# Kernel optimization log

Hardware: AMD Instinct MI355X
Metric: run time of the kernel (lower is better)

The kernel has to match this reference:

```python
import jax, jax.numpy as jnp
import numpy as np

N_NODES = 100000
F_DIM = 128      # graph.num_node_features
TE_DIM = 32      # te_emb_dim
D = F_DIM + TE_DIM  # attention embed_dim = 160
B = 4096         # number of target nodes (batched python loop)
K = 64           # candidates per target
TAU = 1.0
THRESHOLD = 0.2
EPS = 1e-10


def setup_inputs() -> dict:
    key = jax.random.key(0)
    ks = jax.random.split(key, 16)
    inp = {
        "x": jax.random.normal(ks[0], (N_NODES, F_DIM), dtype=jnp.float32),
        "target_node_ids": jax.random.randint(ks[1], (B,), 0, N_NODES),
        "target_node_times": jax.random.randint(ks[2], (B,), 1, 10000),
        "neighbor_ids": jax.random.randint(ks[3], (B, K), 0, N_NODES),
        "edge_time": jax.random.randint(ks[4], (B, K), 0, 10000),
        "edge_weight": jax.random.uniform(ks[5], (B, K), dtype=jnp.float32),
        "gumbel_u": jax.random.uniform(ks[6], (B, K), dtype=jnp.float32),
        # TemporalEncoding params: te(t) = cos(t * w + b)
        "te_w": jax.random.normal(ks[7], (TE_DIM,), dtype=jnp.float32),
        "te_b": jax.random.normal(ks[8], (TE_DIM,), dtype=jnp.float32),
        # MultiheadAttention params (packed qkv like torch)
        "in_proj_w": jax.random.normal(ks[9], (3 * D, D), dtype=jnp.float32) / np.sqrt(D),
        "in_proj_b": jnp.zeros((3 * D,), dtype=jnp.float32),
        "out_w": jax.random.normal(ks[10], (D, D), dtype=jnp.float32) / np.sqrt(D),
        "out_b": jnp.zeros((D,), dtype=jnp.float32),
        # MLP: Linear(D+1 -> 1) + LeakyReLU
        "mlp_w": jax.random.normal(ks[11], (D + 1,), dtype=jnp.float32) / np.sqrt(D + 1),
        "mlp_b": jnp.zeros((1,), dtype=jnp.float32),
    }
    return inp


def reference(x, target_node_ids, target_node_times, neighbor_ids, edge_time,
              edge_weight, gumbel_u, te_w, te_b, in_proj_w, in_proj_b,
              out_w, out_b, mlp_w, mlp_b):
    # --- build target embedding: [B, D]
    t_x = x[target_node_ids]                                          # [B, F]
    t_te = jnp.cos(target_node_times[:, None].astype(jnp.float32) * te_w + te_b)  # [B, TE]
    q_in = jnp.concatenate([t_x, t_te], axis=-1)                      # [B, D]

    # --- candidate embeddings: [B, K, D]
    c_x = x[neighbor_ids]                                             # [B, K, F]
    c_te = jnp.cos(edge_time[..., None].astype(jnp.float32) * te_w + te_b)        # [B, K, TE]
    kv_in = jnp.concatenate([c_x, c_te], axis=-1)                     # [B, K, D]

    # --- single-head MultiheadAttention (eval mode, 1 query per target)
    Wq, Wk, Wv = in_proj_w[:D], in_proj_w[D:2 * D], in_proj_w[2 * D:]
    bq, bk, bv = in_proj_b[:D], in_proj_b[D:2 * D], in_proj_b[2 * D:]
    q = q_in @ Wq.T + bq                                              # [B, D]
    k = jnp.einsum('bkf,df->bkd', kv_in, Wk) + bk                     # [B, K, D]
    v = jnp.einsum('bkf,df->bkd', kv_in, Wv) + bv                     # [B, K, D]
    scores = jnp.einsum('bd,bkd->bk', q, k) / jnp.sqrt(jnp.float32(D))
    attn_w = jax.nn.softmax(scores, axis=-1)                          # [B, K]
    ctx = jnp.einsum('bk,bkd->bd', attn_w, v)                         # [B, D]
    attn_output = ctx @ out_w.T + out_b                               # [B, D]

    # --- gumbel-softmax mask over attention weights (soft, then threshold)
    g = -jnp.log(-jnp.log(gumbel_u + EPS) + EPS)                      # gumbel(0,1)
    y_soft = jax.nn.softmax((attn_w + g) / TAU, axis=-1)
    candidate_mask = y_soft > THRESHOLD                               # [B, K] bool

    # --- MLP edge-weight update: Linear(D+1 -> 1) + LeakyReLU
    mlp_in = jnp.concatenate(
        [jnp.broadcast_to(attn_output[:, None, :], (attn_output.shape[0], edge_weight.shape[1], attn_output.shape[1])),
         edge_weight[..., None]], axis=-1)                            # [B, K, D+1]
    new_edge_weight = jax.nn.leaky_relu(jnp.einsum('bkf,f->bk', mlp_in, mlp_w) + mlp_b[0])  # [B, K]

    return attn_output, new_edge_weight, candidate_mask
```

## Files before the change

kernel.cpp:

```cpp
#include <hip/hip_runtime.h>

#define F_DIM 128
#define TE_DIM 32
#define DD 160
#define NB 4096
#define KK 64
#define ROWS 4
#define LD 164
#define TE_STRIDE 36

#define WS_M   0
#define WS_V2  25600
#define WS_C   51200
#define WS_U   51360
#define WS_B2  51520
#define WS_S0  51680
#define WS_TE  51684
#define TAB_T  10000
#define TAB_N  (TAB_T * TE_DIM)
#define TAB_BLOCKS 250
#define SETUP_BASE (2 * DD + 3)

__device__ __forceinline__ float dot4acc(const float4 w, const float4 v, float a) {
    a = fmaf(w.x, v.x, a);
    a = fmaf(w.y, v.y, a);
    a = fmaf(w.z, v.z, a);
    a = fmaf(w.w, v.w, a);
    return a;
}

__device__ __forceinline__ float wave_max(float v) {
    #pragma unroll
    for (int off = 32; off > 0; off >>= 1) v = fmaxf(v, __shfl_xor(v, off, 64));
    return v;
}
__device__ __forceinline__ float wave_sum(float v) {
    #pragma unroll
    for (int off = 32; off > 0; off >>= 1) v += __shfl_xor(v, off, 64);
    return v;
}

__device__ __forceinline__ void gemv512(
    const float* __restrict__ W, const float* __restrict__ bias,
    const float (*vin)[LD], float (*vout)[LD], int tid)
{
    const int r  = tid & 3;
    const int dl = tid >> 2;
    const float4* v4 = (const float4*)vin[r];
    const float4* w0 = (const float4*)(W + (long)dl * DD);
    float a0 = bias[dl];
    if (dl < 32) {
        const float4* w1 = (const float4*)(W + (long)(dl + 128) * DD);
        float a1 = bias[dl + 128];
        #pragma unroll 8
        for (int f = 0; f < 40; ++f) {
            const float4 v = v4[f];
            a0 = dot4acc(w0[f], v, a0);
            a1 = dot4acc(w1[f], v, a1);
        }
        vout[r][dl]       = a0;
        vout[r][dl + 128] = a1;
    } else {
        #pragma unroll 8
        for (int f = 0; f < 40; ++f) {
            const float4 v = v4[f];
            a0 = dot4acc(w0[f], v, a0);
        }
        vout[r][dl] = a0;
    }
}

__device__ __forceinline__ void gemv512_2(
    const float* __restrict__ W, const float* __restrict__ bias,
    const float (*vin)[2][LD], float (*vout)[LD], int tid)
{
    const int r  = tid & 3;
    const int dl = tid >> 2;
    const float4* va = (const float4*)vin[r][0];
    const float4* vb = (const float4*)vin[r][1];
    const float4* w0 = (const float4*)(W + (long)dl * DD);
    float a0 = bias[dl];
    if (dl < 32) {
        const float4* w1 = (const float4*)(W + (long)(dl + 128) * DD);
        float a1 = bias[dl + 128];
        #pragma unroll 8
        for (int f = 0; f < 40; ++f) {
            const float4 A = va[f], B = vb[f];
            float4 v; v.x = A.x + B.x; v.y = A.y + B.y; v.z = A.z + B.z; v.w = A.w + B.w;
            a0 = dot4acc(w0[f], v, a0);
            a1 = dot4acc(w1[f], v, a1);
        }
        vout[r][dl]       = a0;
        vout[r][dl + 128] = a1;
    } else {
        #pragma unroll 8
        for (int f = 0; f < 40; ++f) {
            const float4 A = va[f], B = vb[f];
            float4 v; v.x = A.x + B.x; v.y = A.y + B.y; v.z = A.z + B.z; v.w = A.w + B.w;
            a0 = dot4acc(w0[f], v, a0);
        }
        vout[r][dl] = a0;
    }
}

__global__ __launch_bounds__(256)
void setup_kernel(const float* __restrict__ ipw, const float* __restrict__ ipb,
                  const float* __restrict__ ow,  const float* __restrict__ ob,
                  const float* __restrict__ te_w, const float* __restrict__ te_b,
                  float* __restrict__ ws)
{
    const int blk = blockIdx.x;
    const int t   = threadIdx.x;
    const float inv = 0.07905694150420949f;

    __shared__ float s_vec[DD];

    if (blk >= SETUP_BASE) {
        const int g0 = (blk - SETUP_BASE) * 256 + t;
        #pragma unroll
        for (int it = 0; it < 5; ++it) {
            const int g = g0 + it * (TAB_BLOCKS * 256);
            const int tt = g >> 5, d = g & 31;
            ws[WS_TE + g] = cosf(fmaf((float)tt, te_w[d], te_b[d]));
        }
        return;
    }

    if (blk < DD) {
        const float* wk = ipw + DD * DD;
        if (t < DD) s_vec[t] = wk[(long)t * DD + blk];
        __syncthreads();
        if (t < DD) {
            float a0 = 0.f, a1 = 0.f, a2 = 0.f, a3 = 0.f;
            #pragma unroll 4
            for (int d = 0; d < DD; d += 4) {
                a0 = fmaf(s_vec[d],     ipw[(long)d * DD + t],       a0);
                a1 = fmaf(s_vec[d + 1], ipw[(long)(d + 1) * DD + t], a1);
                a2 = fmaf(s_vec[d + 2], ipw[(long)(d + 2) * DD + t], a2);
                a3 = fmaf(s_vec[d + 3], ipw[(long)(d + 3) * DD + t], a3);
            }
            ws[WS_M + blk * DD + t] = (a0 + a1 + a2 + a3) * inv;
        }
    } else if (blk < 2 * DD) {
        const int i = blk - DD;
        const float* wv = ipw + 2 * DD * DD;
        if (t < DD) s_vec[t] = ow[(long)i * DD + t];
        __syncthreads();
        if (t < DD) {
            float a0 = 0.f, a1 = 0.f, a2 = 0.f, a3 = 0.f;
            #pragma unroll 4
            for (int d = 0; d < DD; d += 4) {
                a0 = fmaf(s_vec[d],     wv[(long)d * DD + t],       a0);
                a1 = fmaf(s_vec[d + 1], wv[(long)(d + 1) * DD + t], a1);
                a2 = fmaf(s_vec[d + 2], wv[(long)(d + 2) * DD + t], a2);
                a3 = fmaf(s_vec[d + 3], wv[(long)(d + 3) * DD + t], a3);
            }
            ws[WS_V2 + i * DD + t] = a0 + a1 + a2 + a3;
        }
    } else if (blk == 2 * DD) {
        const float* wk = ipw + DD * DD;
        if (t < DD) s_vec[t] = ipb[t];
        __syncthreads();
        if (t < DD) {
            float a0 = 0.f, a1 = 0.f, a2 = 0.f, a3 = 0.f;
            #pragma unroll 4
            for (int d = 0; d < DD; d += 4) {
                a0 = fmaf(s_vec[d],     wk[(long)d * DD + t],       a0);
                a1 = fmaf(s_vec[d + 1], wk[(long)(d + 1) * DD + t], a1);
                a2 = fmaf(s_vec[d + 2], wk[(long)(d + 2) * DD + t], a2);
                a3 = fmaf(s_vec[d + 3], wk[(long)(d + 3) * DD + t], a3);
            }
            ws[WS_C + t] = (a0 + a1 + a2 + a3) * inv;
        }
    } else if (blk == 2 * DD + 1) {
        if (t < DD) s_vec[t] = ipb[DD + t];
        __syncthreads();
        if (t < DD) {
            float a0 = 0.f, a1 = 0.f, a2 = 0.f, a3 = 0.f;
            #pragma unroll 4
            for (int d = 0; d < DD; d += 4) {
                a0 = fmaf(s_vec[d],     ipw[(long)d * DD + t],       a0);
                a1 = fmaf(s_vec[d + 1], ipw[(long)(d + 1) * DD + t], a1);
                a2 = fmaf(s_vec[d + 2], ipw[(long)(d + 2) * DD + t], a2);
                a3 = fmaf(s_vec[d + 3], ipw[(long)(d + 3) * DD + t], a3);
            }
            ws[WS_U + t] = (a0 + a1 + a2 + a3) * inv;
        }
    } else {
        if (t < DD) s_vec[t] = ipb[2 * DD + t];
        __syncthreads();
        if (t < DD) {
            const float* owr = ow + (long)t * DD;
            float a0 = 0.f, a1 = 0.f, a2 = 0.f, a3 = 0.f;
            #pragma unroll 4
            for (int d = 0; d < DD; d += 4) {
                a0 = fmaf(s_vec[d],     owr[d],     a0);
                a1 = fmaf(s_vec[d + 1], owr[d + 1], a1);
                a2 = fmaf(s_vec[d + 2], owr[d + 2], a2);
                a3 = fmaf(s_vec[d + 3], owr[d + 3], a3);
            }
            ws[WS_B2 + t] = ob[t] + (a0 + a1 + a2 + a3);
        }
        if (t >= 192) {
            const int lane = t - 192;
            float p = ipb[lane] * ipb[DD + lane];
            p = fmaf(ipb[lane + 64], ipb[DD + lane + 64], p);
            if (lane < 32) p = fmaf(ipb[lane + 128], ipb[DD + lane + 128], p);
            const float s = wave_sum(p);
            if (lane == 0) ws[WS_S0] = s * inv;
        }
    }
}

__global__ __launch_bounds__(512, 4)
void structure_learner_kernel(
    const float* __restrict__ x,
    const int*   __restrict__ target_node_ids,
    const int*   __restrict__ target_node_times,
    const int*   __restrict__ neighbor_ids,
    const int*   __restrict__ edge_time,
    const float* __restrict__ edge_weight,
    const float* __restrict__ gumbel_u,
    const float* __restrict__ te_w,
    const float* __restrict__ te_b,
    const float* __restrict__ mlp_w,
    const float* __restrict__ mlp_b,
    const float* __restrict__ ws,
    const float* __restrict__ tetab,
    float* __restrict__ out_ao,
    float* __restrict__ out_new,
    float* __restrict__ out_mask)
{
    __shared__ __attribute__((aligned(16))) float s_qin[ROWS][LD];
    __shared__ __attribute__((aligned(16))) float s_qt[ROWS][LD];
    __shared__ __attribute__((aligned(16))) float s_wkvh[ROWS][2][LD];
    __shared__ __attribute__((aligned(16))) float s_ao[ROWS][LD];
    __shared__ float s_scp[ROWS][2][KK];
    __shared__ float s_attnw[ROWS][2][KK];
    __shared__ int   s_nid[ROWS][KK];
    __shared__ __attribute__((aligned(4))) _Float16 s_te[ROWS][KK][TE_STRIDE];

    const int tid  = threadIdx.x;
    const int w    = tid >> 6;
    const int lane = tid & 63;
    const int r    = w >> 1;
    const int h    = w & 1;
    const int b    = blockIdx.x * ROWS + r;

    const float* Mw = ws + WS_M;
    const float* V2 = ws + WS_V2;
    const float* Cv = ws + WS_C;
    const float* Uv = ws + WS_U;
    const float* B2 = ws + WS_B2;
    const float  s0 = ws[WS_S0];

    {
        if (h == 0) {
            s_nid[r][lane] = neighbor_ids[(long)b * KK + lane];
            const int tn = target_node_ids[b];
            const float2 tx = *(const float2*)(x + (long)tn * F_DIM + lane * 2);
            s_qin[r][lane * 2]     = tx.x;
            s_qin[r][lane * 2 + 1] = tx.y;
        } else if (lane < TE_DIM) {
            const int tt = target_node_times[b];
            s_qin[r][F_DIM + lane] =
                (tetab && (unsigned)tt < (unsigned)TAB_T)
                    ? tetab[(long)tt * TE_DIM + lane]
                    : cosf(fmaf((float)tt, te_w[lane], te_b[lane]));
        }
        const int q = lane >> 1, j = lane & 1;
        const int k = 32 * h + q;
        const int etv_i = edge_time[(long)b * KK + k];
        if (tetab && (unsigned)etv_i < (unsigned)TAB_T) {
            const float4* trow = (const float4*)(tetab + (long)etv_i * TE_DIM);
            #pragma unroll
            for (int q4 = 0; q4 < 4; ++q4) {
                const int jj = 4 * j + q4;
                const float4 tv = trow[jj];
                union { _Float16 h2[2]; unsigned u; } p0, p1;
                p0.h2[0] = (_Float16)tv.x; p0.h2[1] = (_Float16)tv.y;
                p1.h2[0] = (_Float16)tv.z; p1.h2[1] = (_Float16)tv.w;
                *(unsigned*)&s_te[r][k][4 * jj]     = p0.u;
                *(unsigned*)&s_te[r][k][4 * jj + 2] = p1.u;
            }
        } else {
            const float etv = (float)etv_i;
            #pragma unroll
            for (int ii = 0; ii < 8; ++ii) {
                const int d0 = 16 * j + 2 * ii;
                union { _Float16 h2[2]; unsigned u; } pk;
                pk.h2[0] = (_Float16)cosf(fmaf(etv, te_w[d0],     te_b[d0]));
                pk.h2[1] = (_Float16)cosf(fmaf(etv, te_w[d0 + 1], te_b[d0 + 1]));
                *(unsigned*)&s_te[r][k][d0] = pk.u;
            }
        }
    }
    __syncthreads();

    gemv512(Mw, Cv, s_qin, s_qt, tid);
    __syncthreads();

    {
        float acc0 = 0.f, acc1 = 0.f;
        const int nidk = s_nid[r][lane];
        const float4* xr  = (const float4*)(x + (long)nidk * F_DIM + 64 * h);
        const float4* qt4 = (const float4*)(s_qt[r] + 64 * h);
        #pragma unroll
        for (int f = 0; f < 16; f += 2) {
            acc0 = dot4acc(xr[f],     qt4[f],     acc0);
            acc1 = dot4acc(xr[f + 1], qt4[f + 1], acc1);
        }
        float acc = acc0 + acc1;
        if (h == 0) {
            const float* qte = s_qt[r] + F_DIM;
            #pragma unroll
            for (int jj = 0; jj < 16; ++jj) {
                union { _Float16 h2[2]; unsigned u; } pk;
                pk.u = *(const unsigned*)&s_te[r][lane][2 * jj];
                acc = fmaf(qte[2 * jj],     (float)pk.h2[0], acc);
                acc = fmaf(qte[2 * jj + 1], (float)pk.h2[1], acc);
            }
            float p = s_qin[r][lane] * Uv[lane];
            p = fmaf(s_qin[r][lane + 64], Uv[lane + 64], p);
            if (lane < 32) p = fmaf(s_qin[r][128 + lane], Uv[128 + lane], p);
            acc += wave_sum(p) + s0;
        }
        s_scp[r][h][lane] = acc;
    }
    __syncthreads();

    float aw;
    {
        const float sc = s_scp[r][0][lane] + s_scp[r][1][lane];
        const float m = wave_max(sc);
        const float e = expf(sc - m);
        const float l = wave_sum(e);
        aw = e / l;
        s_attnw[r][h][lane] = aw;
    }

    {
        float ax = 0.f, ay = 0.f, at = 0.f;
        const float* xb = x + lane * 2;
        const int lte = lane & 31;
        #pragma unroll 8
        for (int qq = 0; qq < 32; ++qq) {
            const int kq = 32 * h + qq;
            const float wgt = s_attnw[r][h][kq];
            const int   nid = s_nid[r][kq];
            const float2 xv = *(const float2*)(xb + (long)nid * F_DIM);
            ax = fmaf(wgt, xv.x, ax);
            ay = fmaf(wgt, xv.y, ay);
            at = fmaf(wgt, (float)s_te[r][kq][lte], at);
        }
        s_wkvh[r][h][lane * 2]     = ax;
        s_wkvh[r][h][lane * 2 + 1] = ay;
        if (lane < TE_DIM) s_wkvh[r][h][F_DIM + lane] = at;
    }
    __syncthreads();

    float u = 0.f, ew = 0.f;
    if (h == 0) {
        u  = gumbel_u[(long)b * KK + lane];
        ew = edge_weight[(long)b * KK + lane];
    }

    gemv512_2(V2, B2, s_wkvh, s_ao, tid);
    __syncthreads();

    if (h == 0) {
        float p = s_ao[r][lane] * mlp_w[lane];
        p = fmaf(s_ao[r][lane + 64], mlp_w[lane + 64], p);
        if (lane < 32) p = fmaf(s_ao[r][lane + 128], mlp_w[lane + 128], p);
        const float base = wave_sum(p) + mlp_b[0];

        float* ao = out_ao + (long)b * DD;
        ao[lane]      = s_ao[r][lane];
        ao[lane + 64] = s_ao[r][lane + 64];
        if (lane < 32) ao[lane + 128] = s_ao[r][lane + 128];

        const float g = -logf(-logf(u + 1e-10f) + 1e-10f);
        const float z = aw + g;
        const float m = wave_max(z);
        const float e = expf(z - m);
        const float l = wave_sum(e);
        out_mask[(long)b * KK + lane] = (e / l > 0.2f) ? 1.0f : 0.0f;

        const float val = fmaf(ew, mlp_w[DD], base);
        out_new[(long)b * KK + lane] = (val >= 0.f) ? val : 0.01f * val;
    }
}

extern "C" void kernel_launch(void* const* d_in, const int* in_sizes, int n_in,
                              void* d_out, int out_size, void* d_ws, size_t ws_size,
                              hipStream_t stream) {
    const float* x   = (const float*)d_in[0];
    const int*   tni = (const int*)d_in[1];
    const int*   tnt = (const int*)d_in[2];
    const int*   nid = (const int*)d_in[3];
    const int*   et  = (const int*)d_in[4];
    const float* ew  = (const float*)d_in[5];
    const float* gu  = (const float*)d_in[6];
    const float* tew = (const float*)d_in[7];
    const float* teb = (const float*)d_in[8];
    const float* ipw = (const float*)d_in[9];
    const float* ipb = (const float*)d_in[10];
    const float* ow  = (const float*)d_in[11];
    const float* ob  = (const float*)d_in[12];
    const float* mw  = (const float*)d_in[13];
    const float* mb  = (const float*)d_in[14];

    float* wsf = (float*)d_ws;

    float* out      = (float*)d_out;
    float* out_ao   = out;
    float* out_new  = out + (long)NB * DD;
    float* out_mask = out + (long)NB * DD + (long)NB * KK;

    const bool use_tab = ws_size >= (size_t)(WS_TE + TAB_N) * sizeof(float);
    const int  setup_grid = SETUP_BASE + (use_tab ? TAB_BLOCKS : 0);

    setup_kernel<<<setup_grid, 256, 0, stream>>>(ipw, ipb, ow, ob, tew, teb, wsf);

    structure_learner_kernel<<<NB / ROWS, 512, 0, stream>>>(
        x, tni, tnt, nid, et, ew, gu, tew, teb, mw, mb, wsf,
        use_tab ? (wsf + WS_TE) : nullptr,
        out_ao, out_new, out_mask);
}
```

Baseline: 178.0 us.

## Cache gathered neighbor rows in LDS as fp16 and halve rows per block

The gathered neighbor feature rows read for the score dot product are now also stored in shared memory as fp16, so the weighted-sum pass reads them from LDS instead of gathering x from global memory a second time. The block shrinks from 4 rows/512 threads to 2 rows/256 threads, and the GEMV thread mapping changes to match. This removes a second random global gather but adds fp16 rounding to the context vector and uses about 33 KB of LDS per block, which may limit occupancy.

```diff
diff --git a/kernel.cpp b/kernel.cpp
--- a/kernel.cpp
+++ b/kernel.cpp
@@ -5,9 +5,10 @@
 #define DD 160
 #define NB 4096
 #define KK 64
-#define ROWS 4
+#define ROWS 2
 #define LD 164
 #define TE_STRIDE 36
+#define XH_STRIDE 132
 
 #define WS_M   0
 #define WS_V2  25600
@@ -40,12 +41,12 @@
     return v;
 }
 
-__device__ __forceinline__ void gemv512(
+__device__ __forceinline__ void gemv2r(
     const float* __restrict__ W, const float* __restrict__ bias,
     const float (*vin)[LD], float (*vout)[LD], int tid)
 {
-    const int r  = tid & 3;
-    const int dl = tid >> 2;
+    const int r  = tid & 1;
+    const int dl = tid >> 1;
     const float4* v4 = (const float4*)vin[r];
     const float4* w0 = (const float4*)(W + (long)dl * DD);
     float a0 = bias[dl];
@@ -70,12 +71,12 @@
     }
 }
 
-__device__ __forceinline__ void gemv512_2(
+__device__ __forceinline__ void gemv2r_sum2(
     const float* __restrict__ W, const float* __restrict__ bias,
     const float (*vin)[2][LD], float (*vout)[LD], int tid)
 {
-    const int r  = tid & 3;
-    const int dl = tid >> 2;
+    const int r  = tid & 1;
+    const int dl = tid >> 1;
     const float4* va = (const float4*)vin[r][0];
     const float4* vb = (const float4*)vin[r][1];
     const float4* w0 = (const float4*)(W + (long)dl * DD);
@@ -212,7 +213,7 @@
     }
 }
 
-__global__ __launch_bounds__(512, 4)
+__global__ __launch_bounds__(256, 4)
 void structure_learner_kernel(
     const float* __restrict__ x,
     const int*   __restrict__ target_node_ids,
@@ -231,6 +232,7 @@
     float* __restrict__ out_new,
     float* __restrict__ out_mask)
 {
+    __shared__ __attribute__((aligned(16))) _Float16 s_xh[ROWS][KK][XH_STRIDE];
     __shared__ __attribute__((aligned(16))) float s_qin[ROWS][LD];
     __shared__ __attribute__((aligned(16))) float s_qt[ROWS][LD];
     __shared__ __attribute__((aligned(16))) float s_wkvh[ROWS][2][LD];
@@ -297,7 +299,7 @@
     }
     __syncthreads();
 
-    gemv512(Mw, Cv, s_qin, s_qt, tid);
+    gemv2r(Mw, Cv, s_qin, s_qt, tid);
     __syncthreads();
 
     {
@@ -305,10 +307,19 @@
         const int nidk = s_nid[r][lane];
         const float4* xr  = (const float4*)(x + (long)nidk * F_DIM + 64 * h);
         const float4* qt4 = (const float4*)(s_qt[r] + 64 * h);
+        _Float16* st = &s_xh[r][lane][64 * h];
         #pragma unroll
         for (int f = 0; f < 16; f += 2) {
-            acc0 = dot4acc(xr[f],     qt4[f],     acc0);
-            acc1 = dot4acc(xr[f + 1], qt4[f + 1], acc1);
+            const float4 a = xr[f], c = xr[f + 1];
+            acc0 = dot4acc(a, qt4[f],     acc0);
+            acc1 = dot4acc(c, qt4[f + 1], acc1);
+            union { _Float16 hh[4]; unsigned long long u; } pa, pb;
+            pa.hh[0] = (_Float16)a.x; pa.hh[1] = (_Float16)a.y;
+            pa.hh[2] = (_Float16)a.z; pa.hh[3] = (_Float16)a.w;
+            pb.hh[0] = (_Float16)c.x; pb.hh[1] = (_Float16)c.y;
+            pb.hh[2] = (_Float16)c.z; pb.hh[3] = (_Float16)c.w;
+            *(unsigned long long*)&st[4 * f]     = pa.u;
+            *(unsigned long long*)&st[4 * f + 4] = pb.u;
         }
         float acc = acc0 + acc1;
         if (h == 0) {
@@ -341,16 +352,15 @@
 
     {
         float ax = 0.f, ay = 0.f, at = 0.f;
-        const float* xb = x + lane * 2;
         const int lte = lane & 31;
         #pragma unroll 8
         for (int qq = 0; qq < 32; ++qq) {
             const int kq = 32 * h + qq;
             const float wgt = s_attnw[r][h][kq];
-            const int   nid = s_nid[r][kq];
-            const float2 xv = *(const float2*)(xb + (long)nid * F_DIM);
-            ax = fmaf(wgt, xv.x, ax);
-            ay = fmaf(wgt, xv.y, ay);
+            union { unsigned u; _Float16 h2[2]; } c;
+            c.u = *(const unsigned*)&s_xh[r][kq][2 * lane];
+            ax = fmaf(wgt, (float)c.h2[0], ax);
+            ay = fmaf(wgt, (float)c.h2[1], ay);
             at = fmaf(wgt, (float)s_te[r][kq][lte], at);
         }
         s_wkvh[r][h][lane * 2]     = ax;
@@ -365,7 +375,7 @@
         ew = edge_weight[(long)b * KK + lane];
     }
 
-    gemv512_2(V2, B2, s_wkvh, s_ao, tid);
+    gemv2r_sum2(V2, B2, s_wkvh, s_ao, tid);
     __syncthreads();
 
     if (h == 0) {
@@ -422,7 +432,7 @@
 
     setup_kernel<<<setup_grid, 256, 0, stream>>>(ipw, ipb, ow, ob, tew, teb, wsf);
 
-    structure_learner_kernel<<<NB / ROWS, 512, 0, stream>>>(
+    structure_learner_kernel<<<NB / ROWS, 256, 0, stream>>>(
         x, tni, tnt, nid, et, ew, gu, tew, teb, mw, mb, wsf,
         use_tab ? (wsf + WS_TE) : nullptr,
         out_ao, out_new, out_mask);
```

After: 181.9 us. 2.2% more time.
